# Kernel tuning notes

Measured on AMD Instinct MI355X. Metric: run time of the kernel, lower is better.

Reference implementation:

```python
import jax, jax.numpy as jnp
import numpy as np

N = 100000      # nodes
E = 3200000     # edges (avg degree 32)
F_IN = 256      # n_features
HID = 128       # n_hidden
C = 16          # n_classes
K = 10          # propagation hops


def setup_inputs() -> dict:
    key = jax.random.key(0)
    ks = jax.random.split(key, 12)
    x = jax.random.normal(ks[0], (N, F_IN), jnp.float32)
    edge_index = jax.random.randint(ks[1], (2, E), 0, N, dtype=jnp.int64)
    edge_attr = jax.random.uniform(ks[2], (E,), jnp.float32)
    # learned parameters (torch Linear layout: W [out, in], b [out])
    def lin(k, fan_out, fan_in):
        s = 1.0 / np.sqrt(fan_in)
        kw, kb = jax.random.split(k)
        W = jax.random.uniform(kw, (fan_out, fan_in), jnp.float32, -s, s)
        b = jax.random.uniform(kb, (fan_out,), jnp.float32, -s, s)
        return W, b
    lin1_w, lin1_b = lin(ks[3], HID, F_IN)
    lin2_w, lin2_b = lin(ks[4], HID, HID)   # hidden lin (n_layers-3 == 1)
    lin3_w, lin3_b = lin(ks[5], C, HID)     # classes lin
    proj_w, proj_b = lin(ks[6], 1, C)       # Prop retain-score projection
    return {"x": x, "edge_index": edge_index, "edge_attr": edge_attr,
            "lin1_w": lin1_w, "lin1_b": lin1_b,
            "lin2_w": lin2_w, "lin2_b": lin2_b,
            "lin3_w": lin3_w, "lin3_b": lin3_b,
            "proj_w": proj_w, "proj_b": proj_b}


def reference(x, edge_index, edge_attr,
              lin1_w, lin1_b, lin2_w, lin2_b, lin3_w, lin3_b,
              proj_w, proj_b):
    # MLP stack (dropout is identity in eval mode)
    h = jax.nn.relu(x @ lin1_w.T + lin1_b)
    h = jax.nn.relu(h @ lin2_w.T + lin2_b)
    h = jax.nn.relu(h @ lin3_w.T + lin3_b)          # [N, C]

    src, dst = edge_index[0], edge_index[1]
    norm = edge_attr[:, None]                        # [E, 1]

    def hop(carry, _):
        msg = norm * carry[src]                      # gather + scale [E, C]
        nxt = jax.ops.segment_sum(msg, dst, num_segments=N)  # scatter-add
        return nxt, nxt

    _, hops = jax.lax.scan(hop, h, None, length=K)   # [K, N, C]
    pps = jnp.concatenate([h[None], hops], axis=0)   # [K+1, N, C]
    pps = jnp.transpose(pps, (1, 0, 2))              # [N, K+1, C]

    # adaptive combination: sigmoid(Linear(C->1)) per hop, weighted sum
    score = jax.nn.sigmoid(jnp.einsum('nkc,c->nk', pps, proj_w[0]) + proj_b[0])
    out = jnp.einsum('nk,nkc->nc', score, pps)       # [N, C]
    return out
```

## Files before the change

kernel.cpp:

```cpp
#include <hip/hip_runtime.h>
#include <hip/hip_bf16.h>
#include <math.h>

#define N_NODES 100000
#define E_EDGES 3200000
#define K_HOPS  10
#define NPP     512
#define NPART   ((N_NODES + NPP - 1) / NPP)
#define CHUNK   8192
#define EPT     (CHUNK / 256)

typedef __attribute__((ext_vector_type(8))) short short8;
typedef __attribute__((ext_vector_type(4))) float floatx4;

__device__ __forceinline__ ushort f2bf(float f) {
    uint u = __float_as_uint(f);
    u += 0x7fffu + ((u >> 16) & 1u);
    return (ushort)(u >> 16);
}
__device__ __forceinline__ uint pk2(float a, float b) {
    return (uint)f2bf(a) | ((uint)f2bf(b) << 16);
}
__device__ __forceinline__ float bflo(uint u) { return __uint_as_float(u << 16); }
__device__ __forceinline__ float bfhi(uint u) { return __uint_as_float(u & 0xffff0000u); }

template<int KD, int MD, bool A_F32>
__global__ __launch_bounds__(256) void mfma_mlp(
    const void* __restrict__ Av, const float* __restrict__ W,
    const float* __restrict__ bias, ushort* __restrict__ C)
{
    constexpr int NCT = MD / 16;
    constexpr int LDW = 88;
    __shared__ ushort Wl[MD * LDW];

    const int t    = threadIdx.x;
    const int w    = t >> 6;
    const int lane = t & 63;
    const int m    = lane & 15;
    const int quad = lane >> 4;
    const int rowBase = blockIdx.x * 128 + w * 32;

    floatx4 acc[2][NCT];
#pragma unroll
    for (int rt = 0; rt < 2; ++rt)
#pragma unroll
        for (int ct = 0; ct < NCT; ++ct) acc[rt][ct] = (floatx4)0.f;

    for (int kb = 0; kb < KD; kb += 64) {
#pragma unroll
        for (int j = 0; j < MD / 16; ++j) {
            int flat = j * 256 + t;
            int n  = flat >> 4;
            int c4 = (flat & 15) * 4;
            floatx4 v = *(const floatx4*)&W[(size_t)n * KD + kb + c4];
            *(uint2*)&Wl[n * LDW + c4] = make_uint2(pk2(v[0], v[1]), pk2(v[2], v[3]));
        }
        __syncthreads();
#pragma unroll
        for (int ks = 0; ks < 64; ks += 32) {
            short8 af[2];
#pragma unroll
            for (int rt = 0; rt < 2; ++rt) {
                int row = rowBase + rt * 16 + m;
                row = row < N_NODES ? row : N_NODES - 1;
                size_t base = (size_t)row * KD + kb + ks + quad * 8;
                if constexpr (A_F32) {
                    const float* ap = (const float*)Av + base;
                    floatx4 a0 = *(const floatx4*)ap;
                    floatx4 a1 = *(const floatx4*)(ap + 4);
                    short8 x;
                    x[0] = (short)f2bf(a0[0]); x[1] = (short)f2bf(a0[1]);
                    x[2] = (short)f2bf(a0[2]); x[3] = (short)f2bf(a0[3]);
                    x[4] = (short)f2bf(a1[0]); x[5] = (short)f2bf(a1[1]);
                    x[6] = (short)f2bf(a1[2]); x[7] = (short)f2bf(a1[3]);
                    af[rt] = x;
                } else {
                    af[rt] = *(const short8*)((const ushort*)Av + base);
                }
            }
#pragma unroll
            for (int ct = 0; ct < NCT; ++ct) {
                short8 bf = *(const short8*)&Wl[(ct * 16 + m) * LDW + ks + quad * 8];
#pragma unroll
                for (int rt = 0; rt < 2; ++rt)
                    acc[rt][ct] = __builtin_amdgcn_mfma_f32_16x16x32_bf16(
                        af[rt], bf, acc[rt][ct], 0, 0, 0);
            }
        }
        __syncthreads();
    }

#pragma unroll
    for (int rt = 0; rt < 2; ++rt) {
#pragma unroll
        for (int r = 0; r < 4; ++r) {
            int row = rowBase + rt * 16 + quad * 4 + r;
            if (row < N_NODES) {
#pragma unroll
                for (int ct = 0; ct < NCT; ++ct) {
                    int col = ct * 16 + m;
                    float v = acc[rt][ct][r] + bias[col];
                    v = v > 0.f ? v : 0.f;
                    C[(size_t)row * MD + col] = f2bf(v);
                }
            }
        }
    }
}

__global__ __launch_bounds__(256) void partition_hist(
    const int* __restrict__ dst, int* __restrict__ pcnt)
{
    __shared__ int lhist[256];
    const int t = threadIdx.x;
    lhist[t] = 0;
    __syncthreads();
    const int base = blockIdx.x * CHUNK;
#pragma unroll
    for (int j = 0; j < EPT; ++j) {
        int i = base + j * 256 + t;
        if (i < E_EDGES) atomicAdd(&lhist[dst[i] >> 9], 1);
    }
    __syncthreads();
    if (lhist[t] > 0) atomicAdd(&pcnt[t], lhist[t]);
}

__global__ __launch_bounds__(256) void partition_scan(
    const int* __restrict__ pcnt, int* __restrict__ pbase, int* __restrict__ pcur)
{
    __shared__ int buf[2][256];
    const int t = threadIdx.x;
    int v = (t < NPART) ? pcnt[t] : 0;
    buf[0][t] = v;
    __syncthreads();
    int cur = 0;
#pragma unroll
    for (int d = 1; d < 256; d <<= 1) {
        int x = buf[cur][t];
        if (t >= d) x += buf[cur][t - d];
        buf[cur ^ 1][t] = x;
        cur ^= 1;
        __syncthreads();
    }
    int incl = buf[cur][t];
    int excl = incl - v;
    if (t < NPART) { pbase[t] = excl; pcur[t] = excl; }
    if (t == NPART - 1) pbase[NPART] = incl;
}

__global__ __launch_bounds__(256) void partition_scatter(
    const int* __restrict__ src, const int* __restrict__ dst,
    const float* __restrict__ ea, int* __restrict__ pcur,
    int4* __restrict__ staging)
{
    __shared__ int lhist[256];
    __shared__ int lbase[256];
    const int t = threadIdx.x;
    lhist[t] = 0;
    __syncthreads();
    const int base = blockIdx.x * CHUNK;
    int d[EPT];
#pragma unroll
    for (int j = 0; j < EPT; ++j) {
        int i = base + j * 256 + t;
        d[j] = (i < E_EDGES) ? dst[i] : -1;
        if (d[j] >= 0) atomicAdd(&lhist[d[j] >> 9], 1);
    }
    __syncthreads();
    int cnt = lhist[t];
    if (cnt > 0) lbase[t] = atomicAdd(&pcur[t], cnt);
    __syncthreads();
    lhist[t] = 0;
    __syncthreads();
#pragma unroll
    for (int j = 0; j < EPT; ++j) {
        if (d[j] >= 0) {
            int i = base + j * 256 + t;
            int p = d[j] >> 9;
            int r = atomicAdd(&lhist[p], 1);
            staging[lbase[p] + r] = make_int4(src[i], __float_as_int(ea[i]), d[j], 0);
        }
    }
}

__global__ __launch_bounds__(256) void partition_build(
    const int4* __restrict__ staging, const int* __restrict__ pbase,
    int* __restrict__ rowp, int2* __restrict__ csr)
{
    __shared__ int ncnt[NPP];
    __shared__ int wsum[4];
    const int p = blockIdx.x;
    const int t = threadIdx.x;
    const int lane = t & 63, wid = t >> 6;
    const int e0 = pbase[p], e1 = pbase[p + 1];
    const int n0 = p * NPP;

    ncnt[2 * t] = 0; ncnt[2 * t + 1] = 0;
    __syncthreads();
    for (int e = e0 + t; e < e1; e += 256)
        atomicAdd(&ncnt[staging[e].z - n0], 1);
    __syncthreads();

    int a = ncnt[2 * t], b = ncnt[2 * t + 1];
    int pairsum = a + b;
    int x = pairsum;
#pragma unroll
    for (int dd = 1; dd < 64; dd <<= 1) {
        int y = __shfl_up(x, dd);
        if (lane >= dd) x += y;
    }
    if (lane == 63) wsum[wid] = x;
    __syncthreads();
    int wbase = 0;
    for (int ww = 0; ww < 4; ++ww) if (ww < wid) wbase += wsum[ww];
    int excl = wbase + x - pairsum;
    __syncthreads();
    ncnt[2 * t]     = e0 + excl;
    ncnt[2 * t + 1] = e0 + excl + a;
    int nA = n0 + 2 * t, nB = n0 + 2 * t + 1;
    if (nA < N_NODES) rowp[nA] = e0 + excl;
    if (nB < N_NODES) rowp[nB] = e0 + excl + a;
    if (p == NPART - 1 && t == 0) rowp[N_NODES] = E_EDGES;
    __syncthreads();

    for (int e = e0 + t; e < e1; e += 256) {
        int4 en = staging[e];
        int pos = atomicAdd(&ncnt[en.z - n0], 1);
        csr[pos] = make_int2(en.x, en.y);
    }
}

__global__ __launch_bounds__(256) void init_out_bf16(
    const ushort* __restrict__ h, const float* __restrict__ pw,
    const float* __restrict__ pb, float* __restrict__ out)
{
    const int t = threadIdx.x;
    const int l = t & 1;
    const int n = blockIdx.x * 128 + (t >> 1);
    if (n >= N_NODES) return;
    uint4 v = *(const uint4*)&h[(size_t)n * 16 + l * 8];
    float a0 = bflo(v.x), a1 = bfhi(v.x), a2 = bflo(v.y), a3 = bfhi(v.y);
    float a4 = bflo(v.z), a5 = bfhi(v.z), a6 = bflo(v.w), a7 = bfhi(v.w);
    float4 p0 = ((const float4*)pw)[l * 2];
    float4 p1 = ((const float4*)pw)[l * 2 + 1];
    float part = a0 * p0.x + a1 * p0.y + a2 * p0.z + a3 * p0.w
               + a4 * p1.x + a5 * p1.y + a6 * p1.z + a7 * p1.w;
    part += __shfl_xor(part, 1);
    float s = 1.f / (1.f + __expf(-(part + pb[0])));
    *(float4*)&out[(size_t)n * 16 + l * 8]     = make_float4(s*a0, s*a1, s*a2, s*a3);
    *(float4*)&out[(size_t)n * 16 + l * 8 + 4] = make_float4(s*a4, s*a5, s*a6, s*a7);
}

__global__ __launch_bounds__(256) void hop_bf16(
    const ushort* __restrict__ prev, ushort* __restrict__ next,
    const int* __restrict__ rowp, const int2* __restrict__ csr,
    const float* __restrict__ pw, const float* __restrict__ pb,
    float* __restrict__ out)
{
    const int t = threadIdx.x;
    const int l = t & 1;
    const int g = (t >> 1) & 7;
    const int n = blockIdx.x * 16 + (t >> 4);
    if (n >= N_NODES) return;
    const int e0 = rowp[n], e1 = rowp[n + 1];
    float a[8];
#pragma unroll
    for (int j = 0; j < 8; ++j) a[j] = 0.f;

    int e = e0 + g;
    for (; e + 8 < e1; e += 16) {
        int2 c0 = csr[e];
        int2 c1 = csr[e + 8];
        float w0 = __int_as_float(c0.y);
        float w1 = __int_as_float(c1.y);
        uint4 v0 = *(const uint4*)&prev[(size_t)c0.x * 16 + l * 8];
        uint4 v1 = *(const uint4*)&prev[(size_t)c1.x * 16 + l * 8];
        a[0] += w0 * bflo(v0.x); a[1] += w0 * bfhi(v0.x);
        a[2] += w0 * bflo(v0.y); a[3] += w0 * bfhi(v0.y);
        a[4] += w0 * bflo(v0.z); a[5] += w0 * bfhi(v0.z);
        a[6] += w0 * bflo(v0.w); a[7] += w0 * bfhi(v0.w);
        a[0] += w1 * bflo(v1.x); a[1] += w1 * bfhi(v1.x);
        a[2] += w1 * bflo(v1.y); a[3] += w1 * bfhi(v1.y);
        a[4] += w1 * bflo(v1.z); a[5] += w1 * bfhi(v1.z);
        a[6] += w1 * bflo(v1.w); a[7] += w1 * bfhi(v1.w);
    }
    if (e < e1) {
        int2 c0 = csr[e];
        float w0 = __int_as_float(c0.y);
        uint4 v0 = *(const uint4*)&prev[(size_t)c0.x * 16 + l * 8];
        a[0] += w0 * bflo(v0.x); a[1] += w0 * bfhi(v0.x);
        a[2] += w0 * bflo(v0.y); a[3] += w0 * bfhi(v0.y);
        a[4] += w0 * bflo(v0.z); a[5] += w0 * bfhi(v0.z);
        a[6] += w0 * bflo(v0.w); a[7] += w0 * bfhi(v0.w);
    }

#pragma unroll
    for (int d = 2; d <= 8; d <<= 1) {
#pragma unroll
        for (int j = 0; j < 8; ++j) a[j] += __shfl_xor(a[j], d);
    }

    float4 p0 = ((const float4*)pw)[l * 2];
    float4 p1 = ((const float4*)pw)[l * 2 + 1];
    float part = a[0]*p0.x + a[1]*p0.y + a[2]*p0.z + a[3]*p0.w
               + a[4]*p1.x + a[5]*p1.y + a[6]*p1.z + a[7]*p1.w;
    part += __shfl_xor(part, 1);
    float s = 1.f / (1.f + __expf(-(part + pb[0])));

    if (g == 0) {
        uint4 nv = make_uint4(pk2(a[0], a[1]), pk2(a[2], a[3]),
                              pk2(a[4], a[5]), pk2(a[6], a[7]));
        *(uint4*)&next[(size_t)n * 16 + l * 8] = nv;
        float4 o0 = *(float4*)&out[(size_t)n * 16 + l * 8];
        float4 o1 = *(float4*)&out[(size_t)n * 16 + l * 8 + 4];
        o0.x += s*a[0]; o0.y += s*a[1]; o0.z += s*a[2]; o0.w += s*a[3];
        o1.x += s*a[4]; o1.y += s*a[5]; o1.z += s*a[6]; o1.w += s*a[7];
        *(float4*)&out[(size_t)n * 16 + l * 8]     = o0;
        *(float4*)&out[(size_t)n * 16 + l * 8 + 4] = o1;
    }
}

extern "C" void kernel_launch(void* const* d_in, const int* in_sizes, int n_in,
                              void* d_out, int out_size, void* d_ws, size_t ws_size,
                              hipStream_t stream)
{
    const float* x  = (const float*)d_in[0];
    const int*   ei = (const int*)d_in[1];
    const float* ea = (const float*)d_in[2];
    const float* w1 = (const float*)d_in[3];
    const float* b1 = (const float*)d_in[4];
    const float* w2 = (const float*)d_in[5];
    const float* b2 = (const float*)d_in[6];
    const float* w3 = (const float*)d_in[7];
    const float* b3 = (const float*)d_in[8];
    const float* pw = (const float*)d_in[9];
    const float* pb = (const float*)d_in[10];
    float* out = (float*)d_out;

    char* ws = (char*)d_ws;
    size_t off = 0;
    char*   region0 = ws + off;           off += (size_t)E_EDGES * 16;
    ushort* pingb = (ushort*)(ws + off);  off += (size_t)N_NODES * 16 * 2;
    ushort* pongb = (ushort*)(ws + off);  off += (size_t)N_NODES * 16 * 2;
    int*    rowp  = (int*)(ws + off);     off += (((size_t)(N_NODES + 1) * 4) + 15) & ~(size_t)15;
    int*    pcnt  = (int*)(ws + off);     off += 256 * 4;
    int*    pbase = (int*)(ws + off);     off += 260 * 4;
    int*    pcur  = (int*)(ws + off);     off += 256 * 4;
    int2*   csr   = (int2*)(ws + off);    off += (size_t)E_EDGES * 8;

    int4*   staging = (int4*)region0;
    ushort* h1b = (ushort*)region0;
    ushort* h2b = (ushort*)(region0 + (size_t)N_NODES * 128 * 2);

    const int* src = ei;
    const int* dst = ei + E_EDGES;

    const dim3 blk(256);
    const int mlpGrid    = (N_NODES + 127) / 128;
    const int nodeGrid16 = (N_NODES + 15) / 16;
    const int chunkGrid  = (E_EDGES + CHUNK - 1) / CHUNK;

    hipMemsetAsync(pcnt, 0, 256 * 4, stream);
    partition_hist<<<chunkGrid, blk, 0, stream>>>(dst, pcnt);
    partition_scan<<<1, blk, 0, stream>>>(pcnt, pbase, pcur);
    partition_scatter<<<chunkGrid, blk, 0, stream>>>(src, dst, ea, pcur, staging);
    partition_build<<<NPART, blk, 0, stream>>>(staging, pbase, rowp, csr);

    mfma_mlp<256, 128, true ><<<mlpGrid, blk, 0, stream>>>(x,   w1, b1, h1b);
    mfma_mlp<128, 128, false><<<mlpGrid, blk, 0, stream>>>(h1b, w2, b2, h2b);
    mfma_mlp<128,  16, false><<<mlpGrid, blk, 0, stream>>>(h2b, w3, b3, pingb);

    init_out_bf16<<<mlpGrid, blk, 0, stream>>>(pingb, pw, pb, out);

    const ushort* prev = pingb;
    ushort* next = pongb;
    for (int k = 0; k < K_HOPS; ++k) {
        hop_bf16<<<nodeGrid16, blk, 0, stream>>>(prev, next, rowp, csr, pw, pb, out);
        ushort* tmp = (ushort*)prev; prev = next; next = tmp;
    }
}
```

Measured before the change: 644.0 us.

## Use per-chunk partition offsets via full matrix scan; shrink hop thread groups

```diff
diff --git a/kernel.cpp b/kernel.cpp
--- a/kernel.cpp
+++ b/kernel.cpp
@@ -5,10 +5,14 @@
 #define N_NODES 100000
 #define E_EDGES 3200000
 #define K_HOPS  10
-#define NPP     512
+#define NPP     256
 #define NPART   ((N_NODES + NPP - 1) / NPP)
-#define CHUNK   8192
+#define CHUNK   4096
 #define EPT     (CHUNK / 256)
+#define NCHUNK  ((E_EDGES + CHUNK - 1) / CHUNK)
+#define NFLAT   (NPART * NCHUNK)
+#define SSEG    8192
+#define GA      ((NFLAT + SSEG - 1) / SSEG)
 
 typedef __attribute__((ext_vector_type(8))) short short8;
 typedef __attribute__((ext_vector_type(4))) float floatx4;
@@ -108,82 +112,132 @@
     }
 }
 
-__global__ __launch_bounds__(256) void partition_hist(
-    const int* __restrict__ dst, int* __restrict__ pcnt)
-{
-    __shared__ int lhist[256];
-    const int t = threadIdx.x;
-    lhist[t] = 0;
+__global__ __launch_bounds__(256) void hist2(
+    const int* __restrict__ dst, int* __restrict__ cmat)
+{
+    __shared__ int lhist[NPART];
+    const int t = threadIdx.x;
+    for (int p = t; p < NPART; p += 256) lhist[p] = 0;
     __syncthreads();
     const int base = blockIdx.x * CHUNK;
 #pragma unroll
     for (int j = 0; j < EPT; ++j) {
         int i = base + j * 256 + t;
-        if (i < E_EDGES) atomicAdd(&lhist[dst[i] >> 9], 1);
-    }
-    __syncthreads();
-    if (lhist[t] > 0) atomicAdd(&pcnt[t], lhist[t]);
-}
-
-__global__ __launch_bounds__(256) void partition_scan(
-    const int* __restrict__ pcnt, int* __restrict__ pbase, int* __restrict__ pcur)
-{
-    __shared__ int buf[2][256];
-    const int t = threadIdx.x;
-    int v = (t < NPART) ? pcnt[t] : 0;
-    buf[0][t] = v;
-    __syncthreads();
-    int cur = 0;
-#pragma unroll
-    for (int d = 1; d < 256; d <<= 1) {
-        int x = buf[cur][t];
-        if (t >= d) x += buf[cur][t - d];
-        buf[cur ^ 1][t] = x;
-        cur ^= 1;
-        __syncthreads();
-    }
-    int incl = buf[cur][t];
-    int excl = incl - v;
-    if (t < NPART) { pbase[t] = excl; pcur[t] = excl; }
-    if (t == NPART - 1) pbase[NPART] = incl;
-}
-
-__global__ __launch_bounds__(256) void partition_scatter(
+        if (i < E_EDGES) atomicAdd(&lhist[dst[i] >> 8], 1);
+    }
+    __syncthreads();
+    for (int p = t; p < NPART; p += 256)
+        cmat[p * NCHUNK + blockIdx.x] = lhist[p];
+}
+
+__global__ __launch_bounds__(1024) void scan_reduce(
+    const int* __restrict__ cmat, int* __restrict__ bsum)
+{
+    __shared__ int wsum[16];
+    const int t = threadIdx.x, lane = t & 63, wid = t >> 6;
+    int base = blockIdx.x * SSEG + t * 8;
+    int s = 0;
+#pragma unroll
+    for (int j = 0; j < 8; ++j) {
+        int idx = base + j;
+        if (idx < NFLAT) s += cmat[idx];
+    }
+#pragma unroll
+    for (int d = 1; d < 64; d <<= 1) s += __shfl_xor(s, d);
+    if (lane == 0) wsum[wid] = s;
+    __syncthreads();
+    if (t == 0) {
+        int tot = 0;
+#pragma unroll
+        for (int i = 0; i < 16; ++i) tot += wsum[i];
+        bsum[blockIdx.x] = tot;
+    }
+}
+
+__global__ void scan_tops(const int* __restrict__ bsum, int* __restrict__ boff)
+{
+    const int t = threadIdx.x;
+    int v = (t < GA) ? bsum[t] : 0;
+    int x = v;
+#pragma unroll
+    for (int d = 1; d < 64; d <<= 1) {
+        int y = __shfl_up(x, d);
+        if (t >= d) x += y;
+    }
+    if (t < GA) boff[t] = x - v;
+}
+
+__global__ __launch_bounds__(1024) void scan_apply(
+    int* __restrict__ cmat, const int* __restrict__ boff, int* __restrict__ pbase)
+{
+    __shared__ int wsum[16];
+    __shared__ int woff[17];
+    const int t = threadIdx.x, lane = t & 63, wid = t >> 6;
+    int base = blockIdx.x * SSEG + t * 8;
+    int v[8], pre[8];
+    int s = 0;
+#pragma unroll
+    for (int j = 0; j < 8; ++j) {
+        int idx = base + j;
+        v[j] = (idx < NFLAT) ? cmat[idx] : 0;
+        pre[j] = s;
+        s += v[j];
+    }
+    int x = s;
+#pragma unroll
+    for (int d = 1; d < 64; d <<= 1) {
+        int y = __shfl_up(x, d);
+        if (lane >= d) x += y;
+    }
+    if (lane == 63) wsum[wid] = x;
+    __syncthreads();
+    if (wid == 0) {
+        int w = (lane < 16) ? wsum[lane] : 0;
+#pragma unroll
+        for (int d = 1; d < 16; d <<= 1) {
+            int y = __shfl_up(w, d);
+            if (lane >= d) w += y;
+        }
+        if (lane < 16) woff[lane + 1] = w;
+        if (lane == 0) woff[0] = 0;
+    }
+    __syncthreads();
+    int tbase = boff[blockIdx.x] + woff[wid] + (x - s);
+#pragma unroll
+    for (int j = 0; j < 8; ++j) {
+        int idx = base + j;
+        if (idx < NFLAT) {
+            int e = tbase + pre[j];
+            cmat[idx] = e;
+            if (idx % NCHUNK == 0) pbase[idx / NCHUNK] = e;
+        }
+    }
+    if (blockIdx.x == 0 && t == 0) pbase[NPART] = E_EDGES;
+}
+
+__global__ __launch_bounds__(256) void scatter2(
     const int* __restrict__ src, const int* __restrict__ dst,
-    const float* __restrict__ ea, int* __restrict__ pcur,
+    const float* __restrict__ ea, const int* __restrict__ cbase,
     int4* __restrict__ staging)
 {
-    __shared__ int lhist[256];
-    __shared__ int lbase[256];
-    const int t = threadIdx.x;
-    lhist[t] = 0;
-    __syncthreads();
-    const int base = blockIdx.x * CHUNK;
-    int d[EPT];
+    __shared__ int lcur[NPART];
+    const int t = threadIdx.x;
+    const int b = blockIdx.x;
+    for (int p = t; p < NPART; p += 256) lcur[p] = cbase[p * NCHUNK + b];
+    __syncthreads();
+    const int base = b * CHUNK;
 #pragma unroll
     for (int j = 0; j < EPT; ++j) {
         int i = base + j * 256 + t;
-        d[j] = (i < E_EDGES) ? dst[i] : -1;
-        if (d[j] >= 0) atomicAdd(&lhist[d[j] >> 9], 1);
-    }
-    __syncthreads();
-    int cnt = lhist[t];
-    if (cnt > 0) lbase[t] = atomicAdd(&pcur[t], cnt);
-    __syncthreads();
-    lhist[t] = 0;
-    __syncthreads();
-#pragma unroll
-    for (int j = 0; j < EPT; ++j) {
-        if (d[j] >= 0) {
-            int i = base + j * 256 + t;
-            int p = d[j] >> 9;
-            int r = atomicAdd(&lhist[p], 1);
-            staging[lbase[p] + r] = make_int4(src[i], __float_as_int(ea[i]), d[j], 0);
-        }
-    }
-}
-
-__global__ __launch_bounds__(256) void partition_build(
+        if (i < E_EDGES) {
+            int d = dst[i];
+            int pos = atomicAdd(&lcur[d >> 8], 1);
+            staging[pos] = make_int4(src[i], __float_as_int(ea[i]), d, 0);
+        }
+    }
+}
+
+__global__ __launch_bounds__(1024) void partition_build(
     const int4* __restrict__ staging, const int* __restrict__ pbase,
     int* __restrict__ rowp, int2* __restrict__ csr)
 {
@@ -191,40 +245,44 @@
     __shared__ int wsum[4];
     const int p = blockIdx.x;
     const int t = threadIdx.x;
-    const int lane = t & 63, wid = t >> 6;
     const int e0 = pbase[p], e1 = pbase[p + 1];
-    const int n0 = p * NPP;
-
-    ncnt[2 * t] = 0; ncnt[2 * t + 1] = 0;
-    __syncthreads();
-    for (int e = e0 + t; e < e1; e += 256)
-        atomicAdd(&ncnt[staging[e].z - n0], 1);
-    __syncthreads();
-
-    int a = ncnt[2 * t], b = ncnt[2 * t + 1];
-    int pairsum = a + b;
-    int x = pairsum;
-#pragma unroll
-    for (int dd = 1; dd < 64; dd <<= 1) {
-        int y = __shfl_up(x, dd);
-        if (lane >= dd) x += y;
-    }
-    if (lane == 63) wsum[wid] = x;
-    __syncthreads();
-    int wbase = 0;
-    for (int ww = 0; ww < 4; ++ww) if (ww < wid) wbase += wsum[ww];
-    int excl = wbase + x - pairsum;
-    __syncthreads();
-    ncnt[2 * t]     = e0 + excl;
-    ncnt[2 * t + 1] = e0 + excl + a;
-    int nA = n0 + 2 * t, nB = n0 + 2 * t + 1;
-    if (nA < N_NODES) rowp[nA] = e0 + excl;
-    if (nB < N_NODES) rowp[nB] = e0 + excl + a;
+    const int cnt = e1 - e0;
+    const int n0 = p << 8;
+
+    if (t < NPP) ncnt[t] = 0;
+    __syncthreads();
+    for (int e = t; e < cnt; e += 1024)
+        atomicAdd(&ncnt[staging[e0 + e].z - n0], 1);
+    __syncthreads();
+
+    int x = 0, v = 0;
+    if (t < NPP) {
+        const int lane = t & 63, wid = t >> 6;
+        v = ncnt[t];
+        x = v;
+#pragma unroll
+        for (int d = 1; d < 64; d <<= 1) {
+            int y = __shfl_up(x, d);
+            if (lane >= d) x += y;
+        }
+        if (lane == 63) wsum[wid] = x;
+    }
+    __syncthreads();
+    if (t < NPP) {
+        const int wid = t >> 6;
+        int wbase = 0;
+#pragma unroll
+        for (int w = 0; w < 4; ++w) if (w < wid) wbase += wsum[w];
+        int excl = wbase + x - v;
+        ncnt[t] = e0 + excl;
+        int n = n0 + t;
+        if (n < N_NODES) rowp[n] = e0 + excl;
+    }
     if (p == NPART - 1 && t == 0) rowp[N_NODES] = E_EDGES;
     __syncthreads();
 
-    for (int e = e0 + t; e < e1; e += 256) {
-        int4 en = staging[e];
+    for (int e = t; e < cnt; e += 1024) {
+        int4 en = staging[e0 + e];
         int pos = atomicAdd(&ncnt[en.z - n0], 1);
         csr[pos] = make_int2(en.x, en.y);
     }
@@ -259,8 +317,8 @@
 {
     const int t = threadIdx.x;
     const int l = t & 1;
-    const int g = (t >> 1) & 7;
-    const int n = blockIdx.x * 16 + (t >> 4);
+    const int g = (t >> 1) & 3;
+    const int n = blockIdx.x * 32 + (t >> 3);
     if (n >= N_NODES) return;
     const int e0 = rowp[n], e1 = rowp[n + 1];
     float a[8];
@@ -268,9 +326,9 @@
     for (int j = 0; j < 8; ++j) a[j] = 0.f;
 
     int e = e0 + g;
-    for (; e + 8 < e1; e += 16) {
+    for (; e + 4 < e1; e += 8) {
         int2 c0 = csr[e];
-        int2 c1 = csr[e + 8];
+        int2 c1 = csr[e + 4];
         float w0 = __int_as_float(c0.y);
         float w1 = __int_as_float(c1.y);
         uint4 v0 = *(const uint4*)&prev[(size_t)c0.x * 16 + l * 8];
@@ -295,7 +353,7 @@
     }
 
 #pragma unroll
-    for (int d = 2; d <= 8; d <<= 1) {
+    for (int d = 2; d <= 4; d <<= 1) {
 #pragma unroll
         for (int j = 0; j < 8; ++j) a[j] += __shfl_xor(a[j], d);
     }
@@ -343,9 +401,10 @@
     ushort* pingb = (ushort*)(ws + off);  off += (size_t)N_NODES * 16 * 2;
     ushort* pongb = (ushort*)(ws + off);  off += (size_t)N_NODES * 16 * 2;
     int*    rowp  = (int*)(ws + off);     off += (((size_t)(N_NODES + 1) * 4) + 15) & ~(size_t)15;
-    int*    pcnt  = (int*)(ws + off);     off += 256 * 4;
-    int*    pbase = (int*)(ws + off);     off += 260 * 4;
-    int*    pcur  = (int*)(ws + off);     off += 256 * 4;
+    int*    cmat  = (int*)(ws + off);     off += ((size_t)NFLAT * 4 + 15) & ~(size_t)15;
+    int*    bsum  = (int*)(ws + off);     off += ((size_t)GA * 4 + 15) & ~(size_t)15;
+    int*    boff  = (int*)(ws + off);     off += ((size_t)GA * 4 + 15) & ~(size_t)15;
+    int*    pbase = (int*)(ws + off);     off += ((size_t)(NPART + 1) * 4 + 15) & ~(size_t)15;
     int2*   csr   = (int2*)(ws + off);    off += (size_t)E_EDGES * 8;
 
     int4*   staging = (int4*)region0;
@@ -357,14 +416,14 @@
 
     const dim3 blk(256);
     const int mlpGrid    = (N_NODES + 127) / 128;
-    const int nodeGrid16 = (N_NODES + 15) / 16;
-    const int chunkGrid  = (E_EDGES + CHUNK - 1) / CHUNK;
-
-    hipMemsetAsync(pcnt, 0, 256 * 4, stream);
-    partition_hist<<<chunkGrid, blk, 0, stream>>>(dst, pcnt);
-    partition_scan<<<1, blk, 0, stream>>>(pcnt, pbase, pcur);
-    partition_scatter<<<chunkGrid, blk, 0, stream>>>(src, dst, ea, pcur, staging);
-    partition_build<<<NPART, blk, 0, stream>>>(staging, pbase, rowp, csr);
+    const int hopGrid    = (N_NODES + 31) / 32;
+
+    hist2<<<NCHUNK, blk, 0, stream>>>(dst, cmat);
+    scan_reduce<<<GA, 1024, 0, stream>>>(cmat, bsum);
+    scan_tops<<<1, 64, 0, stream>>>(bsum, boff);
+    scan_apply<<<GA, 1024, 0, stream>>>(cmat, boff, pbase);
+    scatter2<<<NCHUNK, blk, 0, stream>>>(src, dst, ea, cmat, staging);
+    partition_build<<<NPART, 1024, 0, stream>>>(staging, pbase, rowp, csr);
 
     mfma_mlp<256, 128, true ><<<mlpGrid, blk, 0, stream>>>(x,   w1, b1, h1b);
     mfma_mlp<128, 128, false><<<mlpGrid, blk, 0, stream>>>(h1b, w2, b2, h2b);
@@ -375,7 +434,7 @@
     const ushort* prev = pingb;
     ushort* next = pongb;
     for (int k = 0; k < K_HOPS; ++k) {
-        hop_bf16<<<nodeGrid16, blk, 0, stream>>>(prev, next, rowp, csr, pw, pb, out);
+        hop_bf16<<<hopGrid, blk, 0, stream>>>(prev, next, rowp, csr, pw, pb, out);
         ushort* tmp = (ushort*)prev; prev = next; next = tmp;
     }
 }
```

Measured after the change: 640.2 us. Within noise of the previous version (-0.6%).
